# Performance work log

Measured on AMD Instinct MI355X. Metric: run time of the kernel, lower is better.

Reference implementation:

```python
import jax, jax.numpy as jnp
import numpy as np

N_HEADS = 8
D_EMBED = 512
D_HEAD = D_EMBED // N_HEADS  # used only for the scale factor, as in the source


def setup_inputs() -> dict:
    key = jax.random.key(0)
    k1, k2, k3, k4, k5 = jax.random.split(key, 5)
    B, S, D = 4, 4096, D_EMBED
    s = 1.0 / np.sqrt(D)
    return {
        "x": jax.random.normal(k1, (B, S, D), dtype=jnp.float32),
        "w_in": jax.random.normal(k2, (3 * D, D), dtype=jnp.float32) * s,
        "b_in": jax.random.normal(k3, (3 * D,), dtype=jnp.float32) * 0.01,
        "w_out": jax.random.normal(k4, (D, D), dtype=jnp.float32) * s,
        "b_out": jax.random.normal(k5, (D,), dtype=jnp.float32) * 0.01,
    }


def reference(x, w_in, b_in, w_out, b_out):
    # in_proj: torch Linear y = x @ W.T + b ; chunk into q,k,v along last dim
    qkv = jnp.einsum("bsd,ed->bse", x, w_in) + b_in  # [B,S,3D]
    q, k, v = jnp.split(qkv, 3, axis=-1)  # each [B,S,D]
    # NOTE: source never splits into heads; attention over full d_embed,
    # but scaled by sqrt(d_head) = sqrt(d_embed / n_heads).
    scores = jnp.einsum("bqd,bkd->bqk", q, k) / np.sqrt(D_HEAD)  # [B,S,S]
    weight = jax.nn.softmax(scores, axis=-1)
    out = jnp.einsum("bqk,bkd->bqd", weight, v)  # [B,S,D]
    out = jnp.einsum("bsd,ed->bse", out, w_out) + b_out
    return out
```

## Files before the change

kernel.cpp:

```cpp
#include <hip/hip_runtime.h>

typedef __bf16 bf16x8 __attribute__((ext_vector_type(8)));
typedef float f32x4 __attribute__((ext_vector_type(4)));

#define MFMA16(a, b, c) __builtin_amdgcn_mfma_f32_16x16x32_bf16(a, b, c, 0, 0, 0)
#define LOG2E 1.44269504088896340736f

__device__ __forceinline__ unsigned short f2bf(float f) {
  union { float f; unsigned u; } v; v.f = f;
  return (unsigned short)((v.u + 0x7fffu + ((v.u >> 16) & 1u)) >> 16);
}
__device__ __forceinline__ bf16x8 ld_frag(const unsigned short* p) {
  return *(const bf16x8*)p;
}
__device__ __forceinline__ void gld_lds16(const unsigned short* g, unsigned short* l) {
  __builtin_amdgcn_global_load_lds(
      (const __attribute__((address_space(1))) unsigned int*)(const void*)g,
      (__attribute__((address_space(3))) unsigned int*)(void*)l, 16, 0, 0);
}

__global__ void cvt_f2bf(const float* __restrict__ in,
                         unsigned short* __restrict__ out, int n4) {
  int i = blockIdx.x * blockDim.x + threadIdx.x;
  if (i < n4) {
    float4 v = ((const float4*)in)[i];
    ushort4 o;
    o.x = f2bf(v.x); o.y = f2bf(v.y); o.z = f2bf(v.z); o.w = f2bf(v.w);
    ((ushort4*)out)[i] = o;
  }
}

__global__ void gemm_bt(const unsigned short* __restrict__ A,
                        const unsigned short* __restrict__ B,
                        const float* __restrict__ bias,
                        float* __restrict__ outf,
                        unsigned short* __restrict__ qbuf,
                        unsigned short* __restrict__ kbuf,
                        unsigned short* __restrict__ vtbuf,
                        int M, int N, int K, int mode) {
  __shared__ alignas(16) unsigned short As[128 * 32];
  __shared__ alignas(16) unsigned short Bs[128 * 32];
  const int n0 = blockIdx.x * 128, m0 = blockIdx.y * 128;
  const int tid = threadIdx.x;
  const int l = tid & 63, w = tid >> 6;
  const int quad = l >> 4, c = l & 15;
  const int wm = (w >> 1) * 64, wn = (w & 1) * 64;

  f32x4 acc[4][4] = {};
  const int kiters = K >> 5;
  for (int kt = 0; kt < kiters; ++kt) {
    __syncthreads();
    const int kk = kt * 32 + (l & 3) * 8;
    const int row = l >> 2;
#pragma unroll
    for (int i = 0; i < 2; ++i) {
      const int rbase = i * 64 + w * 16;
      gld_lds16(&A[(size_t)(m0 + rbase + row) * K + kk], &As[rbase * 32]);
      gld_lds16(&B[(size_t)(n0 + rbase + row) * K + kk], &Bs[rbase * 32]);
    }
    __syncthreads();
    bf16x8 af[4], bfr[4];
#pragma unroll
    for (int t = 0; t < 4; ++t) {
      af[t] = ld_frag(&As[(wm + t * 16 + c) * 32 + quad * 8]);
      bfr[t] = ld_frag(&Bs[(wn + t * 16 + c) * 32 + quad * 8]);
    }
#pragma unroll
    for (int mt = 0; mt < 4; ++mt)
#pragma unroll
      for (int nt = 0; nt < 4; ++nt)
        acc[mt][nt] = MFMA16(af[mt], bfr[nt], acc[mt][nt]);
  }

#pragma unroll
  for (int nt = 0; nt < 4; ++nt) {
    const int n = n0 + wn + nt * 16 + c;
    const float bsum = bias[n];
#pragma unroll
    for (int mt = 0; mt < 4; ++mt) {
      const int mbase = m0 + wm + mt * 16 + quad * 4;
      if (mode == 0) {
#pragma unroll
        for (int r = 0; r < 4; ++r)
          outf[(size_t)(mbase + r) * N + n] = acc[mt][nt][r] + bsum;
      } else if (n < 1024) {
        unsigned short* dst = (n < 512) ? qbuf : kbuf;
        const int nn = n & 511;
#pragma unroll
        for (int r = 0; r < 4; ++r)
          dst[(size_t)(mbase + r) * 512 + nn] = f2bf(acc[mt][nt][r] + bsum);
      } else {
        const int d = n - 1024;
        const int bb = mbase >> 12, s = mbase & 4095;
        ushort4 pk;
        pk.x = f2bf(acc[mt][nt][0] + bsum);
        pk.y = f2bf(acc[mt][nt][1] + bsum);
        pk.z = f2bf(acc[mt][nt][2] + bsum);
        pk.w = f2bf(acc[mt][nt][3] + bsum);
        *(ushort4*)&vtbuf[((size_t)bb * 512 + d) * 4096 + s] = pk;
      }
    }
  }
}

#define KROW 520
#define PROW 40

__global__ __launch_bounds__(256, 2) void attn_kernel(
    const unsigned short* __restrict__ Q, const unsigned short* __restrict__ Kb,
    const unsigned short* __restrict__ Vt, unsigned short* __restrict__ part0,
    unsigned short* __restrict__ part1, float2* __restrict__ mlbuf) {
  __shared__ alignas(16) unsigned short k_lds[32 * KROW];
  __shared__ alignas(16) unsigned short v_lds[512 * 32];
  __shared__ alignas(16) unsigned short p_lds[4 * 16 * PROW];

  const int bid = blockIdx.x;
  const int xcd = bid & 7;
  const int b = xcd >> 1;
  const int half = (bid >> 3) & 1;
  const int qt = (bid >> 4) | ((xcd & 1) << 5);
  const int s0 = qt * 64;
  const int kvbase = half * 2048;
  const int tid = threadIdx.x;
  const int l = tid & 63, w = tid >> 6;
  const int quad = l >> 4, c = l & 15;
  const size_t boff = (size_t)b * 4096 * 512;

  bf16x8 qf[16];
  {
    const unsigned short* qrow = Q + boff + (size_t)(s0 + w * 16 + c) * 512;
#pragma unroll
    for (int ks = 0; ks < 16; ++ks) qf[ks] = ld_frag(&qrow[ks * 32 + quad * 8]);
  }

  f32x4 o[32] = {};
  float m_run = -1e30f, l_run = 0.f;

  const unsigned short* Kbase = Kb + boff;
  const unsigned short* Vbase = Vt + (size_t)b * 512 * 4096;

  auto stage = [&](int kv0) {
#pragma unroll
    for (int i = 0; i < 8; ++i) {
      const int row = i * 4 + w;
      gld_lds16(&Kbase[(size_t)(kv0 + row) * 512 + l * 8], &k_lds[row * KROW]);
    }
#pragma unroll
    for (int i = 0; i < 8; ++i) {
      const int dbase = (i * 4 + w) * 16;
      const int d = dbase + (l >> 2);
      const int jl = (l & 3) ^ ((d >> 1) & 3);
      gld_lds16(&Vbase[(size_t)d * 4096 + kv0 + jl * 8], &v_lds[dbase * 32]);
    }
  };

  for (int it = 0; it < 64; ++it) {
    __syncthreads();
    stage(kvbase + it * 32);
    __syncthreads();

    f32x4 sa[2][2] = {};
#pragma unroll
    for (int ks = 0; ks < 16; ++ks) {
      const unsigned short* kr = &k_lds[c * KROW + ks * 32 + quad * 8];
      bf16x8 kf0 = ld_frag(kr);
      bf16x8 kf1 = ld_frag(kr + 16 * KROW);
      sa[0][ks & 1] = MFMA16(kf0, qf[ks], sa[0][ks & 1]);
      sa[1][ks & 1] = MFMA16(kf1, qf[ks], sa[1][ks & 1]);
    }
    const f32x4 s0v = sa[0][0] + sa[0][1];
    const f32x4 s1v = sa[1][0] + sa[1][1];

    const float C1 = 0.125f * LOG2E;
    float m8 = fmaxf(fmaxf(fmaxf(s0v[0], s0v[1]), fmaxf(s0v[2], s0v[3])),
                     fmaxf(fmaxf(s1v[0], s1v[1]), fmaxf(s1v[2], s1v[3])));
    m8 = fmaxf(m8, __shfl_xor(m8, 16));
    m8 = fmaxf(m8, __shfl_xor(m8, 32));
    const float mn = fmaxf(m_run, m8);

    float p0[4], p1[4], s8 = 0.f;
#pragma unroll
    for (int r = 0; r < 4; ++r) {
      p0[r] = exp2f((s0v[r] - mn) * C1);
      p1[r] = exp2f((s1v[r] - mn) * C1);
      s8 += p0[r] + p1[r];
    }
    unsigned short* prow = &p_lds[(w * 16 + c) * PROW];
    ushort4 pk0, pk1;
    pk0.x = f2bf(p0[0]); pk0.y = f2bf(p0[1]); pk0.z = f2bf(p0[2]); pk0.w = f2bf(p0[3]);
    pk1.x = f2bf(p1[0]); pk1.y = f2bf(p1[1]); pk1.z = f2bf(p1[2]); pk1.w = f2bf(p1[3]);
    *(ushort4*)&prow[quad * 4] = pk0;
    *(ushort4*)&prow[16 + quad * 4] = pk1;

    s8 += __shfl_xor(s8, 16);
    s8 += __shfl_xor(s8, 32);

    if (__any(mn > m_run)) {
      const float alpha = exp2f((m_run - mn) * C1);
      l_run = l_run * alpha + s8;
      m_run = mn;
#pragma unroll
      for (int t = 0; t < 32; ++t) o[t] *= alpha;
    } else {
      l_run += s8;
    }

    asm volatile("s_waitcnt lgkmcnt(0)" ::: "memory");

    const bf16x8 pf = ld_frag(&p_lds[(w * 16 + c) * PROW + quad * 8]);
#pragma unroll
    for (int t = 0; t < 32; ++t) {
      const int d = t * 16 + c;
      const int jp = quad ^ ((d >> 1) & 3);
      bf16x8 vf = ld_frag(&v_lds[d * 32 + jp * 8]);
      o[t] = MFMA16(vf, pf, o[t]);
    }
  }

  unsigned short* part = half ? part1 : part0;
  const float inv = 1.0f / l_run;
  unsigned short* orow = part + boff + (size_t)(s0 + w * 16 + c) * 512;
#pragma unroll
  for (int t = 0; t < 32; ++t) {
    ushort4 pk;
    pk.x = f2bf(o[t][0] * inv);
    pk.y = f2bf(o[t][1] * inv);
    pk.z = f2bf(o[t][2] * inv);
    pk.w = f2bf(o[t][3] * inv);
    *(ushort4*)&orow[t * 16 + quad * 4] = pk;
  }
  if (quad == 0) {
    float2 ml; ml.x = m_run; ml.y = l_run;
    mlbuf[(size_t)half * 16384 + b * 4096 + s0 + w * 16 + c] = ml;
  }
}

__global__ void merge_halves(const unsigned short* __restrict__ p1,
                             const float2* __restrict__ mlbuf,
                             unsigned short* __restrict__ p0out) {
  const int i = blockIdx.x * blockDim.x + threadIdx.x;
  const int row = i >> 6;
  const float2 a = mlbuf[row];
  const float2 bb = mlbuf[16384 + row];
  const float C1 = 0.125f * LOG2E;
  const float M = fmaxf(a.x, bb.x);
  float w0 = a.y * exp2f((a.x - M) * C1);
  float w1 = bb.y * exp2f((bb.x - M) * C1);
  const float inv = 1.0f / (w0 + w1);
  w0 *= inv; w1 *= inv;
  bf16x8 v0 = *(const bf16x8*)(p0out + (size_t)i * 8);
  bf16x8 v1 = *(const bf16x8*)(p1 + (size_t)i * 8);
  ushort4 o0, o1;
  o0.x = f2bf(w0 * (float)v0[0] + w1 * (float)v1[0]);
  o0.y = f2bf(w0 * (float)v0[1] + w1 * (float)v1[1]);
  o0.z = f2bf(w0 * (float)v0[2] + w1 * (float)v1[2]);
  o0.w = f2bf(w0 * (float)v0[3] + w1 * (float)v1[3]);
  o1.x = f2bf(w0 * (float)v0[4] + w1 * (float)v1[4]);
  o1.y = f2bf(w0 * (float)v0[5] + w1 * (float)v1[5]);
  o1.z = f2bf(w0 * (float)v0[6] + w1 * (float)v1[6]);
  o1.w = f2bf(w0 * (float)v0[7] + w1 * (float)v1[7]);
  *(ushort4*)(p0out + (size_t)i * 8) = o0;
  *(ushort4*)(p0out + (size_t)i * 8 + 4) = o1;
}

extern "C" void kernel_launch(void* const* d_in, const int* in_sizes, int n_in,
                              void* d_out, int out_size, void* d_ws, size_t ws_size,
                              hipStream_t stream) {
  const float* x = (const float*)d_in[0];
  const float* w_in = (const float*)d_in[1];
  const float* b_in = (const float*)d_in[2];
  const float* w_out = (const float*)d_in[3];
  const float* b_out = (const float*)d_in[4];
  float* out = (float*)d_out;

  const size_t MTOT = (size_t)4 * 4096 * 512;
  unsigned short* q = (unsigned short*)d_ws;
  unsigned short* k = q + MTOT;
  unsigned short* vt = k + MTOT;
  unsigned short* xbf = vt + MTOT;
  unsigned short* part1 = xbf + MTOT;
  unsigned short* w_in_bf = part1 + MTOT;
  unsigned short* w_out_bf = w_in_bf + 1536 * 512;
  float2* mlbuf = (float2*)(w_out_bf + 512 * 512);

  cvt_f2bf<<<dim3((int)(MTOT / 4 / 256)), 256, 0, stream>>>(x, xbf,
                                                            (int)(MTOT / 4));
  cvt_f2bf<<<dim3(768), 256, 0, stream>>>(w_in, w_in_bf, 1536 * 512 / 4);
  cvt_f2bf<<<dim3(256), 256, 0, stream>>>(w_out, w_out_bf, 512 * 512 / 4);

  gemm_bt<<<dim3(12, 128), 256, 0, stream>>>(xbf, w_in_bf, b_in, nullptr, q, k,
                                             vt, 16384, 1536, 512, 1);
  attn_kernel<<<dim3(512), 256, 0, stream>>>(q, k, vt, xbf, part1, mlbuf);
  merge_halves<<<dim3(4096), 256, 0, stream>>>(part1, mlbuf, xbf);
  gemm_bt<<<dim3(4, 128), 256, 0, stream>>>(xbf, w_out_bf, b_out, out, nullptr,
                                            nullptr, nullptr, 16384, 512, 512,
                                            0);
}
```

Measured before the change: 432.3 us.

## Switch attention kernel to 32x32 MFMA with split-D QK and LDS score reduction

The attention kernel moves from 16x16x32 to 32x32x16 bf16 MFMA tiles. Each pair of waves now splits the 512-wide head dimension for QK^T, and the partial scores are summed through an LDS exchange that reuses the K buffer. The PV product is split across waves by output columns. This raises MFMA tile size and cuts LDS fragment reloads per flop, but adds extra __syncthreads and an LDS round-trip for the score reduction on every iteration.

Measured after the change: 551.0 us. +27.5%, slower.

```diff
diff --git a/kernel.cpp b/kernel.cpp
--- a/kernel.cpp
+++ b/kernel.cpp
@@ -2,8 +2,10 @@
 
 typedef __bf16 bf16x8 __attribute__((ext_vector_type(8)));
 typedef float f32x4 __attribute__((ext_vector_type(4)));
+typedef float f32x16 __attribute__((ext_vector_type(16)));
 
 #define MFMA16(a, b, c) __builtin_amdgcn_mfma_f32_16x16x32_bf16(a, b, c, 0, 0, 0)
+#define MFMA32(a, b, c) __builtin_amdgcn_mfma_f32_32x32x16_bf16(a, b, c, 0, 0, 0)
 #define LOG2E 1.44269504088896340736f
 
 __device__ __forceinline__ unsigned short f2bf(float f) {
@@ -112,7 +114,7 @@
     unsigned short* __restrict__ part1, float2* __restrict__ mlbuf) {
   __shared__ alignas(16) unsigned short k_lds[32 * KROW];
   __shared__ alignas(16) unsigned short v_lds[512 * 32];
-  __shared__ alignas(16) unsigned short p_lds[4 * 16 * PROW];
+  __shared__ alignas(16) unsigned short p_lds[64 * PROW];
 
   const int bid = blockIdx.x;
   const int xcd = bid & 7;
@@ -123,115 +125,143 @@
   const int kvbase = half * 2048;
   const int tid = threadIdx.x;
   const int l = tid & 63, w = tid >> 6;
-  const int quad = l >> 4, c = l & 15;
+  const int qh = w >> 1, kh = w & 1;
+  const int l31 = l & 31, h = l >> 5;
   const size_t boff = (size_t)b * 4096 * 512;
 
   bf16x8 qf[16];
   {
-    const unsigned short* qrow = Q + boff + (size_t)(s0 + w * 16 + c) * 512;
-#pragma unroll
-    for (int ks = 0; ks < 16; ++ks) qf[ks] = ld_frag(&qrow[ks * 32 + quad * 8]);
-  }
-
-  f32x4 o[32] = {};
+    const unsigned short* qrow =
+        Q + boff + (size_t)(s0 + qh * 32 + l31) * 512 + kh * 256 + h * 8;
+#pragma unroll
+    for (int t = 0; t < 16; ++t) qf[t] = ld_frag(&qrow[t * 16]);
+  }
+
+  f32x16 o[8] = {};
   float m_run = -1e30f, l_run = 0.f;
 
   const unsigned short* Kbase = Kb + boff;
   const unsigned short* Vbase = Vt + (size_t)b * 512 * 4096;
-
-  auto stage = [&](int kv0) {
-#pragma unroll
-    for (int i = 0; i < 8; ++i) {
-      const int row = i * 4 + w;
-      gld_lds16(&Kbase[(size_t)(kv0 + row) * 512 + l * 8], &k_lds[row * KROW]);
-    }
-#pragma unroll
-    for (int i = 0; i < 8; ++i) {
-      const int dbase = (i * 4 + w) * 16;
-      const int d = dbase + (l >> 2);
-      const int jl = (l & 3) ^ ((d >> 1) & 3);
-      gld_lds16(&Vbase[(size_t)d * 4096 + kv0 + jl * 8], &v_lds[dbase * 32]);
-    }
-  };
+  f32x4* exv = (f32x4*)k_lds;
 
   for (int it = 0; it < 64; ++it) {
     __syncthreads();
-    stage(kvbase + it * 32);
-    __syncthreads();
-
-    f32x4 sa[2][2] = {};
-#pragma unroll
-    for (int ks = 0; ks < 16; ++ks) {
-      const unsigned short* kr = &k_lds[c * KROW + ks * 32 + quad * 8];
-      bf16x8 kf0 = ld_frag(kr);
-      bf16x8 kf1 = ld_frag(kr + 16 * KROW);
-      sa[0][ks & 1] = MFMA16(kf0, qf[ks], sa[0][ks & 1]);
-      sa[1][ks & 1] = MFMA16(kf1, qf[ks], sa[1][ks & 1]);
-    }
-    const f32x4 s0v = sa[0][0] + sa[0][1];
-    const f32x4 s1v = sa[1][0] + sa[1][1];
+    {
+      const int kv0 = kvbase + it * 32;
+#pragma unroll
+      for (int i = 0; i < 8; ++i) {
+        const int row = i * 4 + w;
+        gld_lds16(&Kbase[(size_t)(kv0 + row) * 512 + l * 8], &k_lds[row * KROW]);
+      }
+#pragma unroll
+      for (int i = 0; i < 8; ++i) {
+        const int dbase = (i * 4 + w) * 16;
+        const int d = dbase + (l >> 2);
+        const int jl = (l & 3) ^ ((d >> 1) & 3);
+        gld_lds16(&Vbase[(size_t)d * 4096 + kv0 + jl * 8], &v_lds[dbase * 32]);
+      }
+    }
+    __syncthreads();
+
+    f32x16 acc0 = {}, acc1 = {};
+#pragma unroll
+    for (int t = 0; t < 16; t += 2) {
+      bf16x8 kf0 = ld_frag(&k_lds[l31 * KROW + (kh * 16 + t) * 16 + h * 8]);
+      bf16x8 kf1 = ld_frag(&k_lds[l31 * KROW + (kh * 16 + t + 1) * 16 + h * 8]);
+      acc0 = MFMA32(kf0, qf[t], acc0);
+      acc1 = MFMA32(kf1, qf[t + 1], acc1);
+    }
+    f32x16 ss = acc0 + acc1;
+    __syncthreads();
+
+#pragma unroll
+    for (int r4 = 0; r4 < 4; ++r4) {
+      f32x4 t4;
+      t4[0] = ss[r4 * 4 + 0]; t4[1] = ss[r4 * 4 + 1];
+      t4[2] = ss[r4 * 4 + 2]; t4[3] = ss[r4 * 4 + 3];
+      exv[(w * 4 + r4) * 64 + l] = t4;
+    }
+    __syncthreads();
+    {
+      const int pw = w ^ 1;
+#pragma unroll
+      for (int r4 = 0; r4 < 4; ++r4) {
+        f32x4 t4 = exv[(pw * 4 + r4) * 64 + l];
+        ss[r4 * 4 + 0] += t4[0]; ss[r4 * 4 + 1] += t4[1];
+        ss[r4 * 4 + 2] += t4[2]; ss[r4 * 4 + 3] += t4[3];
+      }
+    }
 
     const float C1 = 0.125f * LOG2E;
-    float m8 = fmaxf(fmaxf(fmaxf(s0v[0], s0v[1]), fmaxf(s0v[2], s0v[3])),
-                     fmaxf(fmaxf(s1v[0], s1v[1]), fmaxf(s1v[2], s1v[3])));
-    m8 = fmaxf(m8, __shfl_xor(m8, 16));
+    float m8 = ss[0];
+#pragma unroll
+    for (int r = 1; r < 16; ++r) m8 = fmaxf(m8, ss[r]);
     m8 = fmaxf(m8, __shfl_xor(m8, 32));
     const float mn = fmaxf(m_run, m8);
 
-    float p0[4], p1[4], s8 = 0.f;
-#pragma unroll
-    for (int r = 0; r < 4; ++r) {
-      p0[r] = exp2f((s0v[r] - mn) * C1);
-      p1[r] = exp2f((s1v[r] - mn) * C1);
-      s8 += p0[r] + p1[r];
-    }
-    unsigned short* prow = &p_lds[(w * 16 + c) * PROW];
-    ushort4 pk0, pk1;
-    pk0.x = f2bf(p0[0]); pk0.y = f2bf(p0[1]); pk0.z = f2bf(p0[2]); pk0.w = f2bf(p0[3]);
-    pk1.x = f2bf(p1[0]); pk1.y = f2bf(p1[1]); pk1.z = f2bf(p1[2]); pk1.w = f2bf(p1[3]);
-    *(ushort4*)&prow[quad * 4] = pk0;
-    *(ushort4*)&prow[16 + quad * 4] = pk1;
-
-    s8 += __shfl_xor(s8, 16);
+    float p[16], s8 = 0.f;
+#pragma unroll
+    for (int r = 0; r < 16; ++r) {
+      p[r] = exp2f((ss[r] - mn) * C1);
+      s8 += p[r];
+    }
     s8 += __shfl_xor(s8, 32);
+
+    {
+      unsigned short* prow = &p_lds[(qh * 32 + l31) * PROW];
+      const int rb = kh * 8;
+      ushort4 a4, b4;
+      a4.x = f2bf(p[rb + 0]); a4.y = f2bf(p[rb + 1]);
+      a4.z = f2bf(p[rb + 2]); a4.w = f2bf(p[rb + 3]);
+      b4.x = f2bf(p[rb + 4]); b4.y = f2bf(p[rb + 5]);
+      b4.z = f2bf(p[rb + 6]); b4.w = f2bf(p[rb + 7]);
+      *(ushort4*)&prow[kh * 16 + 4 * h] = a4;
+      *(ushort4*)&prow[kh * 16 + 8 + 4 * h] = b4;
+    }
 
     if (__any(mn > m_run)) {
       const float alpha = exp2f((m_run - mn) * C1);
       l_run = l_run * alpha + s8;
       m_run = mn;
 #pragma unroll
-      for (int t = 0; t < 32; ++t) o[t] *= alpha;
+      for (int t = 0; t < 8; ++t)
+#pragma unroll
+        for (int e = 0; e < 16; ++e) o[t][e] *= alpha;
     } else {
       l_run += s8;
     }
-
-    asm volatile("s_waitcnt lgkmcnt(0)" ::: "memory");
-
-    const bf16x8 pf = ld_frag(&p_lds[(w * 16 + c) * PROW + quad * 8]);
-#pragma unroll
-    for (int t = 0; t < 32; ++t) {
-      const int d = t * 16 + c;
-      const int jp = quad ^ ((d >> 1) & 3);
-      bf16x8 vf = ld_frag(&v_lds[d * 32 + jp * 8]);
-      o[t] = MFMA16(vf, pf, o[t]);
+    __syncthreads();
+
+    const bf16x8 pf0 = ld_frag(&p_lds[(qh * 32 + l31) * PROW + h * 8]);
+    const bf16x8 pf1 = ld_frag(&p_lds[(qh * 32 + l31) * PROW + 16 + h * 8]);
+#pragma unroll
+    for (int dt = 0; dt < 8; ++dt) {
+      const int d = kh * 256 + dt * 32 + l31;
+      const int sw = (d >> 1) & 3;
+      bf16x8 vf0 = ld_frag(&v_lds[d * 32 + (h ^ sw) * 8]);
+      bf16x8 vf1 = ld_frag(&v_lds[d * 32 + ((2 + h) ^ sw) * 8]);
+      o[dt] = MFMA32(vf0, pf0, o[dt]);
+      o[dt] = MFMA32(vf1, pf1, o[dt]);
     }
   }
 
   unsigned short* part = half ? part1 : part0;
   const float inv = 1.0f / l_run;
-  unsigned short* orow = part + boff + (size_t)(s0 + w * 16 + c) * 512;
-#pragma unroll
-  for (int t = 0; t < 32; ++t) {
-    ushort4 pk;
-    pk.x = f2bf(o[t][0] * inv);
-    pk.y = f2bf(o[t][1] * inv);
-    pk.z = f2bf(o[t][2] * inv);
-    pk.w = f2bf(o[t][3] * inv);
-    *(ushort4*)&orow[t * 16 + quad * 4] = pk;
-  }
-  if (quad == 0) {
+  unsigned short* orow = part + boff + (size_t)(s0 + qh * 32 + l31) * 512;
+#pragma unroll
+  for (int dt = 0; dt < 8; ++dt)
+#pragma unroll
+    for (int g = 0; g < 4; ++g) {
+      ushort4 pk;
+      pk.x = f2bf(o[dt][g * 4 + 0] * inv);
+      pk.y = f2bf(o[dt][g * 4 + 1] * inv);
+      pk.z = f2bf(o[dt][g * 4 + 2] * inv);
+      pk.w = f2bf(o[dt][g * 4 + 3] * inv);
+      *(ushort4*)&orow[kh * 256 + dt * 32 + g * 8 + 4 * h] = pk;
+    }
+  if (kh == 0 && l < 32) {
     float2 ml; ml.x = m_run; ml.y = l_run;
-    mlbuf[(size_t)half * 16384 + b * 4096 + s0 + w * 16 + c] = ml;
+    mlbuf[(size_t)half * 16384 + b * 4096 + s0 + qh * 32 + l] = ml;
   }
 }
 
```
